# Kernel optimization log

Measured on AMD Instinct MI355X. Metric: run time of the kernel, lower is better.

The kernel has to match this reference:

```python
import jax, jax.numpy as jnp
import numpy as np

N_NODES = 50000
N_EDGES = 800000
IN_F = 256
HID = 64
N_CLASSES = 32
LEAKY_SLOPE = 0.2


def _gat_layer(x, src, dst, W, a_src, a_dst):
    # Standard single-head GAT (GraphAttentionLayer_P0 semantics):
    # h = x W; e_ij = LeakyReLU(a_src.h_j + a_dst.h_i); softmax over in-edges of i;
    # out_i = sum_j alpha_ij h_j
    h = x @ W                                        # [N, F']
    alpha_s = h @ a_src                              # [N]
    alpha_d = h @ a_dst                              # [N]
    e = jax.nn.leaky_relu(alpha_s[src] + alpha_d[dst], LEAKY_SLOPE)  # [E]
    # segment softmax over edges grouped by destination node
    m = jax.ops.segment_max(e, dst, num_segments=N_NODES)           # [N]
    m = jnp.where(jnp.isfinite(m), m, 0.0)            # empty segments -> -inf
    ex = jnp.exp(e - m[dst])                          # [E]
    denom = jax.ops.segment_sum(ex, dst, num_segments=N_NODES)       # [N]
    denom = jnp.where(denom == 0.0, 1.0, denom)
    alpha = ex / denom[dst]                           # [E]
    out = jax.ops.segment_sum(alpha[:, None] * h[src], dst, num_segments=N_NODES)
    return out                                        # [N, F']


def setup_inputs() -> dict:
    key = jax.random.key(0)
    ks = jax.random.split(key, 8)
    x = jax.random.normal(ks[0], (N_NODES, IN_F), dtype=jnp.float32)
    edge_index = jax.random.randint(ks[1], (2, N_EDGES), 0, N_NODES, dtype=jnp.int64)
    s1 = 1.0 / np.sqrt(IN_F)
    s2 = 1.0 / np.sqrt(HID)
    W1 = jax.random.uniform(ks[2], (IN_F, HID), jnp.float32, -s1, s1)
    a1_src = jax.random.uniform(ks[3], (HID,), jnp.float32, -s2, s2)
    a1_dst = jax.random.uniform(ks[4], (HID,), jnp.float32, -s2, s2)
    W2 = jax.random.uniform(ks[5], (HID, N_CLASSES), jnp.float32, -s2, s2)
    s3 = 1.0 / np.sqrt(N_CLASSES)
    a2_src = jax.random.uniform(ks[6], (N_CLASSES,), jnp.float32, -s3, s3)
    a2_dst = jax.random.uniform(ks[7], (N_CLASSES,), jnp.float32, -s3, s3)
    return {"x": x, "edge_index": edge_index, "W1": W1, "a1_src": a1_src,
            "a1_dst": a1_dst, "W2": W2, "a2_src": a2_src, "a2_dst": a2_dst}


def reference(x, edge_index, W1, a1_src, a1_dst, W2, a2_src, a2_dst):
    src, dst = edge_index[0], edge_index[1]
    h = _gat_layer(x, src, dst, W1, a1_src, a1_dst)
    h = jax.nn.relu(h)
    out = _gat_layer(h, src, dst, W2, a2_src, a2_dst)
    return out
```

## Files before the change

kernel.cpp:

```cpp
#include <hip/hip_runtime.h>
#include <math.h>

#define NN 50000
#define NE 800000
#define INF_DIM 256
#define HIDF 64
#define NC 32
#define SLOPE 0.2f


__global__ void k_zero(int* __restrict__ counts){
  int i = blockIdx.x*blockDim.x + threadIdx.x;
  if(i < NN) counts[i] = 0;
}

__global__ void k_hist(const int* __restrict__ dst, int* __restrict__ counts){
  int e = blockIdx.x*blockDim.x + threadIdx.x;
  if(e < NE) atomicAdd(&counts[dst[e]], 1);
}

__global__ void k_scan_a(const int* __restrict__ counts, int* __restrict__ rowstart,
                         int* __restrict__ blocksums){
  __shared__ int wsum[4];
  int tid = threadIdx.x;
  int idx = blockIdx.x*1024 + tid*4;
  int v0 = (idx+0<NN)?counts[idx+0]:0;
  int v1 = (idx+1<NN)?counts[idx+1]:0;
  int v2 = (idx+2<NN)?counts[idx+2]:0;
  int v3 = (idx+3<NN)?counts[idx+3]:0;
  int s0=v0, s1=s0+v1, s2=s1+v2, s3=s2+v3;
  int lane = tid & 63, w = tid >> 6;
  int x = s3;
  #pragma unroll
  for(int off=1; off<64; off<<=1){
    int y = __shfl_up(x, off, 64);
    if(lane >= off) x += y;
  }
  if(lane==63) wsum[w] = x;
  __syncthreads();
  int woff = 0;
  for(int i=0;i<w;i++) woff += wsum[i];
  int excl = woff + (x - s3);
  if(idx+0<NN) rowstart[idx+1] = excl + s0;
  if(idx+1<NN) rowstart[idx+2] = excl + s1;
  if(idx+2<NN) rowstart[idx+3] = excl + s2;
  if(idx+3<NN) rowstart[idx+4] = excl + s3;
  if(tid==0) blocksums[blockIdx.x] = wsum[0]+wsum[1]+wsum[2]+wsum[3];
}

__global__ void k_scan_b(const int* __restrict__ blocksums, int* __restrict__ blockoff){
  int lane = threadIdx.x;
  const int nb = (NN + 1023)/1024;
  int v = (lane<nb)? blocksums[lane] : 0;
  int x = v;
  #pragma unroll
  for(int off=1; off<64; off<<=1){
    int y = __shfl_up(x, off, 64);
    if(lane >= off) x += y;
  }
  if(lane<nb) blockoff[lane] = x - v;
}

__global__ void k_scan_c(const int* __restrict__ counts, int* __restrict__ rowstart,
                         const int* __restrict__ blockoff, int* __restrict__ cursor){
  int i = blockIdx.x*blockDim.x + threadIdx.x;
  if(i < NN){
    int incl = rowstart[i+1] + blockoff[i>>10];
    rowstart[i+1] = incl;
    cursor[i] = incl - counts[i];
    if(i==0) rowstart[0] = 0;
  }
}

__global__ void k_scatter(const int* __restrict__ src, const int* __restrict__ dst,
                          int* __restrict__ cursor, int* __restrict__ ssrc){
  int e = blockIdx.x*blockDim.x + threadIdx.x;
  if(e < NE){
    int d = dst[e];
    int pos = atomicAdd(&cursor[d], 1);
    ssrc[pos] = src[e];
  }
}

#define LDXS 20

__global__ __launch_bounds__(64) void k_gemm1(
    const float* __restrict__ x, const float* __restrict__ W,
    const float* __restrict__ a_s, const float* __restrict__ a_d,
    float* __restrict__ h, float* __restrict__ as_o, float* __restrict__ ad_o){
  __shared__ float xs[64*LDXS];
  __shared__ float ws[16*64];
  int tid = threadIdx.x;
  int ng = tid >> 3;
  int cg = tid & 7;
  int nb0 = blockIdx.x*64;

  int srow = nb0 + tid; if(srow > NN-1) srow = NN-1;
  const float* xrow = x + (size_t)srow*INF_DIM;
  int wrow = tid >> 2;
  int wcol = (tid & 3)*16;

  float4 xr[4], wr[4];
  #pragma unroll
  for(int j=0;j<4;j++){
    xr[j] = *reinterpret_cast<const float4*>(xrow + j*4);
    wr[j] = *reinterpret_cast<const float4*>(W + wrow*64 + wcol + j*4);
  }

  float4 acc0[8], acc1[8];
  #pragma unroll
  for(int i=0;i<8;i++){
    acc0[i] = make_float4(0.f,0.f,0.f,0.f);
    acc1[i] = make_float4(0.f,0.f,0.f,0.f);
  }

  for(int kt=0; kt<16; ++kt){
    #pragma unroll
    for(int j=0;j<4;j++){
      *reinterpret_cast<float4*>(xs + tid*LDXS + j*4) = xr[j];
      *reinterpret_cast<float4*>(ws + wrow*64 + wcol + j*4) = wr[j];
    }
    __syncthreads();
    if(kt < 15){
      #pragma unroll
      for(int j=0;j<4;j++){
        xr[j] = *reinterpret_cast<const float4*>(xrow + (kt+1)*16 + j*4);
        wr[j] = *reinterpret_cast<const float4*>(W + ((kt+1)*16 + wrow)*64 + wcol + j*4);
      }
    }
    #pragma unroll
    for(int k4=0;k4<4;k4++){
      int k = k4*4;
      float4 wa[4], wb[4];
      #pragma unroll
      for(int kk=0;kk<4;kk++){
        wa[kk] = *reinterpret_cast<const float4*>(ws + (k+kk)*64 + cg*8);
        wb[kk] = *reinterpret_cast<const float4*>(ws + (k+kk)*64 + cg*8 + 4);
      }
      #pragma unroll
      for(int i=0;i<8;i++){
        float4 xv = *reinterpret_cast<const float4*>(xs + (ng + 8*i)*LDXS + k);
        acc0[i].x += xv.x*wa[0].x + xv.y*wa[1].x + xv.z*wa[2].x + xv.w*wa[3].x;
        acc0[i].y += xv.x*wa[0].y + xv.y*wa[1].y + xv.z*wa[2].y + xv.w*wa[3].y;
        acc0[i].z += xv.x*wa[0].z + xv.y*wa[1].z + xv.z*wa[2].z + xv.w*wa[3].z;
        acc0[i].w += xv.x*wa[0].w + xv.y*wa[1].w + xv.z*wa[2].w + xv.w*wa[3].w;
        acc1[i].x += xv.x*wb[0].x + xv.y*wb[1].x + xv.z*wb[2].x + xv.w*wb[3].x;
        acc1[i].y += xv.x*wb[0].y + xv.y*wb[1].y + xv.z*wb[2].y + xv.w*wb[3].y;
        acc1[i].z += xv.x*wb[0].z + xv.y*wb[1].z + xv.z*wb[2].z + xv.w*wb[3].z;
        acc1[i].w += xv.x*wb[0].w + xv.y*wb[1].w + xv.z*wb[2].w + xv.w*wb[3].w;
      }
    }
    __syncthreads();
  }

  float4 asA = *reinterpret_cast<const float4*>(a_s + cg*8);
  float4 asB = *reinterpret_cast<const float4*>(a_s + cg*8 + 4);
  float4 adA = *reinterpret_cast<const float4*>(a_d + cg*8);
  float4 adB = *reinterpret_cast<const float4*>(a_d + cg*8 + 4);
  #pragma unroll
  for(int i=0;i<8;i++){
    int n = nb0 + ng + 8*i;
    float sv = acc0[i].x*asA.x + acc0[i].y*asA.y + acc0[i].z*asA.z + acc0[i].w*asA.w
             + acc1[i].x*asB.x + acc1[i].y*asB.y + acc1[i].z*asB.z + acc1[i].w*asB.w;
    float dv = acc0[i].x*adA.x + acc0[i].y*adA.y + acc0[i].z*adA.z + acc0[i].w*adA.w
             + acc1[i].x*adB.x + acc1[i].y*adB.y + acc1[i].z*adB.z + acc1[i].w*adB.w;
    #pragma unroll
    for(int mk=1; mk<8; mk<<=1){
      sv += __shfl_xor(sv, mk, 64);
      dv += __shfl_xor(dv, mk, 64);
    }
    if(n < NN){
      *reinterpret_cast<float4*>(h + (size_t)n*HIDF + cg*8)     = acc0[i];
      *reinterpret_cast<float4*>(h + (size_t)n*HIDF + cg*8 + 4) = acc1[i];
      if(cg==0){ as_o[n]=sv; ad_o[n]=dv; }
    }
  }
}


__global__ __launch_bounds__(256) void k_agg1(
    const float* __restrict__ h1, const float* __restrict__ as1, const float* __restrict__ ad1,
    const int* __restrict__ rowstart, const int* __restrict__ ssrc,
    float* __restrict__ r1){
  int wv = threadIdx.x >> 6;
  int lane = threadIdx.x & 63;
  int n = blockIdx.x*4 + wv;
  int rs = rowstart[n], re = rowstart[n+1];
  float adn = ad1[n];
  float m = -1e30f, l = 0.f, acc = 0.f;
  for(int base=rs; base<re; base+=64){
    int cnt = re - base; if(cnt > 64) cnt = 64;
    int s = 0; float z = -1e30f;
    if(lane < cnt){
      s = ssrc[base+lane];
      float zz = as1[s] + adn;
      z = zz > 0.f ? zz : SLOPE*zz;
    }
    float cm = z;
    #pragma unroll
    for(int off=32; off>=1; off>>=1) cm = fmaxf(cm, __shfl_xor(cm, off, 64));
    float nm = fmaxf(m, cm);
    float sc = __expf(m - nm);
    float p = (lane<cnt) ? __expf(z - nm) : 0.f;
    float cs = p;
    #pragma unroll
    for(int off=32; off>=1; off>>=1) cs += __shfl_xor(cs, off, 64);
    l = l*sc + cs;
    acc *= sc;
    for(int e=0; e<cnt; ++e){
      int   se = __shfl(s, e, 64);
      float pe = __shfl(p, e, 64);
      acc += pe * h1[(size_t)se*HIDF + lane];
    }
    m = nm;
  }
  float o = (l > 0.f) ? acc/l : 0.f;
  r1[(size_t)n*HIDF + lane] = fmaxf(o, 0.f);
}


__global__ __launch_bounds__(64) void k_gemm2(
    const float* __restrict__ r1, const float* __restrict__ W2,
    const float* __restrict__ a_s, const float* __restrict__ a_d,
    float* __restrict__ h2, float* __restrict__ as_o, float* __restrict__ ad_o){
  __shared__ float ws2[64*32];
  int tid = threadIdx.x;
  int ng = tid >> 2;
  int cg = tid & 3;
  int nb0 = blockIdx.x*128;
  #pragma unroll
  for(int j=0;j<8;j++)
    *reinterpret_cast<float4*>(ws2 + tid*32 + j*4) =
        *reinterpret_cast<const float4*>(W2 + tid*32 + j*4);
  __syncthreads();

  float4 acc0[8], acc1[8];
  #pragma unroll
  for(int i=0;i<8;i++){
    acc0[i] = make_float4(0.f,0.f,0.f,0.f);
    acc1[i] = make_float4(0.f,0.f,0.f,0.f);
  }

  float4 xc[8], xn[8];
  #pragma unroll
  for(int i=0;i<8;i++){
    int n = nb0 + ng + 16*i; if(n > NN-1) n = NN-1;
    xc[i] = *reinterpret_cast<const float4*>(r1 + (size_t)n*HIDF);
  }
  for(int k4=0;k4<16;k4++){
    if(k4 < 15){
      #pragma unroll
      for(int i=0;i<8;i++){
        int n = nb0 + ng + 16*i; if(n > NN-1) n = NN-1;
        xn[i] = *reinterpret_cast<const float4*>(r1 + (size_t)n*HIDF + (k4+1)*4);
      }
    }
    float4 wa[4], wb[4];
    #pragma unroll
    for(int kk=0;kk<4;kk++){
      wa[kk] = *reinterpret_cast<const float4*>(ws2 + (k4*4+kk)*32 + cg*8);
      wb[kk] = *reinterpret_cast<const float4*>(ws2 + (k4*4+kk)*32 + cg*8 + 4);
    }
    #pragma unroll
    for(int i=0;i<8;i++){
      float4 xv = xc[i];
      acc0[i].x += xv.x*wa[0].x + xv.y*wa[1].x + xv.z*wa[2].x + xv.w*wa[3].x;
      acc0[i].y += xv.x*wa[0].y + xv.y*wa[1].y + xv.z*wa[2].y + xv.w*wa[3].y;
      acc0[i].z += xv.x*wa[0].z + xv.y*wa[1].z + xv.z*wa[2].z + xv.w*wa[3].z;
      acc0[i].w += xv.x*wa[0].w + xv.y*wa[1].w + xv.z*wa[2].w + xv.w*wa[3].w;
      acc1[i].x += xv.x*wb[0].x + xv.y*wb[1].x + xv.z*wb[2].x + xv.w*wb[3].x;
      acc1[i].y += xv.x*wb[0].y + xv.y*wb[1].y + xv.z*wb[2].y + xv.w*wb[3].y;
      acc1[i].z += xv.x*wb[0].z + xv.y*wb[1].z + xv.z*wb[2].z + xv.w*wb[3].z;
      acc1[i].w += xv.x*wb[0].w + xv.y*wb[1].w + xv.z*wb[2].w + xv.w*wb[3].w;
    }
    #pragma unroll
    for(int i=0;i<8;i++) xc[i] = xn[i];
  }

  float4 asA = *reinterpret_cast<const float4*>(a_s + cg*8);
  float4 asB = *reinterpret_cast<const float4*>(a_s + cg*8 + 4);
  float4 adA = *reinterpret_cast<const float4*>(a_d + cg*8);
  float4 adB = *reinterpret_cast<const float4*>(a_d + cg*8 + 4);
  #pragma unroll
  for(int i=0;i<8;i++){
    int n = nb0 + ng + 16*i;
    float sv = acc0[i].x*asA.x + acc0[i].y*asA.y + acc0[i].z*asA.z + acc0[i].w*asA.w
             + acc1[i].x*asB.x + acc1[i].y*asB.y + acc1[i].z*asB.z + acc1[i].w*asB.w;
    float dv = acc0[i].x*adA.x + acc0[i].y*adA.y + acc0[i].z*adA.z + acc0[i].w*adA.w
             + acc1[i].x*adB.x + acc1[i].y*adB.y + acc1[i].z*adB.z + acc1[i].w*adB.w;
    #pragma unroll
    for(int mk=1; mk<4; mk<<=1){
      sv += __shfl_xor(sv, mk, 64);
      dv += __shfl_xor(dv, mk, 64);
    }
    if(n < NN){
      *reinterpret_cast<float4*>(h2 + (size_t)n*NC + cg*8)     = acc0[i];
      *reinterpret_cast<float4*>(h2 + (size_t)n*NC + cg*8 + 4) = acc1[i];
      if(cg==0){ as_o[n]=sv; ad_o[n]=dv; }
    }
  }
}


__global__ __launch_bounds__(256) void k_agg2(
    const float* __restrict__ h2, const float* __restrict__ as2, const float* __restrict__ ad2,
    const int* __restrict__ rowstart, const int* __restrict__ ssrc,
    float* __restrict__ out){
  int tid = threadIdx.x;
  int sub = tid >> 5;
  int c = tid & 31;
  int n = blockIdx.x*8 + sub;
  int rs = rowstart[n], re = rowstart[n+1];
  float adn = ad2[n];
  float m = -1e30f, l = 0.f, acc = 0.f;
  for(int base=rs; base<re; base+=32){
    int cnt = re - base; if(cnt > 32) cnt = 32;
    int s = 0; float z = -1e30f;
    if(c < cnt){
      s = ssrc[base+c];
      float zz = as2[s] + adn;
      z = zz > 0.f ? zz : SLOPE*zz;
    }
    float cm = z;
    #pragma unroll
    for(int off=16; off>=1; off>>=1) cm = fmaxf(cm, __shfl_xor(cm, off, 32));
    float nm = fmaxf(m, cm);
    float sc = __expf(m - nm);
    float p = (c<cnt) ? __expf(z - nm) : 0.f;
    float cs = p;
    #pragma unroll
    for(int off=16; off>=1; off>>=1) cs += __shfl_xor(cs, off, 32);
    l = l*sc + cs;
    acc *= sc;
    for(int e=0; e<cnt; ++e){
      int   se = __shfl(s, e, 32);
      float pe = __shfl(p, e, 32);
      acc += pe * h2[(size_t)se*NC + c];
    }
    m = nm;
  }
  out[(size_t)n*NC + c] = (l > 0.f) ? acc/l : 0.f;
}


extern "C" void kernel_launch(void* const* d_in, const int* in_sizes, int n_in,
                              void* d_out, int out_size, void* d_ws, size_t ws_size,
                              hipStream_t stream){
  const float* x   = (const float*)d_in[0];
  const int*   ei  = (const int*)d_in[1];
  const float* W1  = (const float*)d_in[2];
  const float* a1s = (const float*)d_in[3];
  const float* a1d = (const float*)d_in[4];
  const float* W2  = (const float*)d_in[5];
  const float* a2s = (const float*)d_in[6];
  const float* a2d = (const float*)d_in[7];
  const int* srcIdx = ei;
  const int* dstIdx = ei + NE;
  float* out = (float*)d_out;

  char* wsp = (char*)d_ws;
  size_t off = 0;
  auto alloc = [&](size_t bytes)->void*{
    void* p = wsp + off;
    off = (off + bytes + 255) & ~(size_t)255;
    return p;
  };
  int* counts    = (int*)alloc((size_t)NN*sizeof(int));
  int* rowstart  = (int*)alloc((size_t)(NN+1)*sizeof(int));
  int* cursor    = (int*)alloc((size_t)NN*sizeof(int));
  int* blocksums = (int*)alloc(64*sizeof(int));
  int* blockoff  = (int*)alloc(64*sizeof(int));
  int* ssrc      = (int*)alloc((size_t)NE*sizeof(int));
  float* h1      = (float*)alloc((size_t)NN*HIDF*sizeof(float));
  float* as1     = (float*)alloc((size_t)NN*sizeof(float));
  float* ad1     = (float*)alloc((size_t)NN*sizeof(float));
  float* r1      = (float*)alloc((size_t)NN*HIDF*sizeof(float));
  float* h2  = h1;
  float* as2 = as1;
  float* ad2 = ad1;

  k_zero   <<<(NN+255)/256, 256, 0, stream>>>(counts);
  k_hist   <<<(NE+255)/256, 256, 0, stream>>>(dstIdx, counts);
  k_scan_a <<<(NN+1023)/1024, 256, 0, stream>>>(counts, rowstart, blocksums);
  k_scan_b <<<1, 64, 0, stream>>>(blocksums, blockoff);
  k_scan_c <<<(NN+255)/256, 256, 0, stream>>>(counts, rowstart, blockoff, cursor);
  k_scatter<<<(NE+255)/256, 256, 0, stream>>>(srcIdx, dstIdx, cursor, ssrc);

  k_gemm1<<<(NN+63)/64, 64, 0, stream>>>(x, W1, a1s, a1d, h1, as1, ad1);
  k_agg1 <<<NN/4, 256, 0, stream>>>(h1, as1, ad1, rowstart, ssrc, r1);

  k_gemm2<<<(NN+127)/128, 64, 0, stream>>>(r1, W2, a2s, a2d, h2, as2, ad2);
  k_agg2 <<<NN/8, 256, 0, stream>>>(h2, as2, ad2, rowstart, ssrc, out);
}
```

Before: 362.5 us.

## Use one-row-per-thread GEMMs with uniform weight loads; stage edge pairs in LDS

Both projection GEMMs are rewritten so each thread computes a full output row, reading weights through wave-uniform global loads instead of staging x and W tiles in shared memory with barriers. The attention dot products are then done in-thread with no shuffles. In the aggregation kernels, the per-edge (source, weight) pairs are written to shared memory and read back as broadcasts, replacing two cross-lane shuffles per edge. The risks are uncoalesced strided row loads of x (each lane reads a different 1 KB row), high register pressure from 64 accumulators, and a missing barrier. The LDS write and reads happen within a single wavefront, so this relies on wave-level ordering.

Measured after the change: 351.5 us. -3.1%, faster.

```diff
diff --git a/kernel.cpp b/kernel.cpp
--- a/kernel.cpp
+++ b/kernel.cpp
@@ -82,98 +82,65 @@
   }
 }
 
-#define LDXS 20
 
 __global__ __launch_bounds__(64) void k_gemm1(
     const float* __restrict__ x, const float* __restrict__ W,
     const float* __restrict__ a_s, const float* __restrict__ a_d,
     float* __restrict__ h, float* __restrict__ as_o, float* __restrict__ ad_o){
-  __shared__ float xs[64*LDXS];
-  __shared__ float ws[16*64];
-  int tid = threadIdx.x;
-  int ng = tid >> 3;
-  int cg = tid & 7;
-  int nb0 = blockIdx.x*64;
-
-  int srow = nb0 + tid; if(srow > NN-1) srow = NN-1;
-  const float* xrow = x + (size_t)srow*INF_DIM;
-  int wrow = tid >> 2;
-  int wcol = (tid & 3)*16;
-
-  float4 xr[4], wr[4];
-  #pragma unroll
-  for(int j=0;j<4;j++){
-    xr[j] = *reinterpret_cast<const float4*>(xrow + j*4);
-    wr[j] = *reinterpret_cast<const float4*>(W + wrow*64 + wcol + j*4);
-  }
-
-  float4 acc0[8], acc1[8];
-  #pragma unroll
-  for(int i=0;i<8;i++){
-    acc0[i] = make_float4(0.f,0.f,0.f,0.f);
-    acc1[i] = make_float4(0.f,0.f,0.f,0.f);
-  }
+  int lane = threadIdx.x;
+  int n = blockIdx.x*64 + lane;
+  int nr = (n < NN) ? n : (NN-1);
+  const float* xrow = x + (size_t)nr*INF_DIM;
+  const float4* Wv = reinterpret_cast<const float4*>(W);
+
+  float4 acc[16];
+  #pragma unroll
+  for(int i=0;i<16;i++) acc[i] = make_float4(0.f,0.f,0.f,0.f);
+
+  float4 xc[4], xn[4];
+  #pragma unroll
+  for(int j=0;j<4;j++) xc[j] = *reinterpret_cast<const float4*>(xrow + j*4);
 
   for(int kt=0; kt<16; ++kt){
-    #pragma unroll
-    for(int j=0;j<4;j++){
-      *reinterpret_cast<float4*>(xs + tid*LDXS + j*4) = xr[j];
-      *reinterpret_cast<float4*>(ws + wrow*64 + wcol + j*4) = wr[j];
-    }
-    __syncthreads();
     if(kt < 15){
       #pragma unroll
-      for(int j=0;j<4;j++){
-        xr[j] = *reinterpret_cast<const float4*>(xrow + (kt+1)*16 + j*4);
-        wr[j] = *reinterpret_cast<const float4*>(W + ((kt+1)*16 + wrow)*64 + wcol + j*4);
+      for(int j=0;j<4;j++)
+        xn[j] = *reinterpret_cast<const float4*>(xrow + (kt+1)*16 + j*4);
+    }
+    #pragma unroll
+    for(int k4=0;k4<4;k4++){
+      int kbase = kt*16 + k4*4;
+      float4 xk = xc[k4];
+      #pragma unroll
+      for(int cb=0;cb<16;cb++){
+        float4 w0 = Wv[(kbase+0)*16 + cb];
+        float4 w1 = Wv[(kbase+1)*16 + cb];
+        float4 w2 = Wv[(kbase+2)*16 + cb];
+        float4 w3 = Wv[(kbase+3)*16 + cb];
+        acc[cb].x += xk.x*w0.x + xk.y*w1.x + xk.z*w2.x + xk.w*w3.x;
+        acc[cb].y += xk.x*w0.y + xk.y*w1.y + xk.z*w2.y + xk.w*w3.y;
+        acc[cb].z += xk.x*w0.z + xk.y*w1.z + xk.z*w2.z + xk.w*w3.z;
+        acc[cb].w += xk.x*w0.w + xk.y*w1.w + xk.z*w2.w + xk.w*w3.w;
       }
     }
     #pragma unroll
-    for(int k4=0;k4<4;k4++){
-      int k = k4*4;
-      float4 wa[4], wb[4];
-      #pragma unroll
-      for(int kk=0;kk<4;kk++){
-        wa[kk] = *reinterpret_cast<const float4*>(ws + (k+kk)*64 + cg*8);
-        wb[kk] = *reinterpret_cast<const float4*>(ws + (k+kk)*64 + cg*8 + 4);
-      }
-      #pragma unroll
-      for(int i=0;i<8;i++){
-        float4 xv = *reinterpret_cast<const float4*>(xs + (ng + 8*i)*LDXS + k);
-        acc0[i].x += xv.x*wa[0].x + xv.y*wa[1].x + xv.z*wa[2].x + xv.w*wa[3].x;
-        acc0[i].y += xv.x*wa[0].y + xv.y*wa[1].y + xv.z*wa[2].y + xv.w*wa[3].y;
-        acc0[i].z += xv.x*wa[0].z + xv.y*wa[1].z + xv.z*wa[2].z + xv.w*wa[3].z;
-        acc0[i].w += xv.x*wa[0].w + xv.y*wa[1].w + xv.z*wa[2].w + xv.w*wa[3].w;
-        acc1[i].x += xv.x*wb[0].x + xv.y*wb[1].x + xv.z*wb[2].x + xv.w*wb[3].x;
-        acc1[i].y += xv.x*wb[0].y + xv.y*wb[1].y + xv.z*wb[2].y + xv.w*wb[3].y;
-        acc1[i].z += xv.x*wb[0].z + xv.y*wb[1].z + xv.z*wb[2].z + xv.w*wb[3].z;
-        acc1[i].w += xv.x*wb[0].w + xv.y*wb[1].w + xv.z*wb[2].w + xv.w*wb[3].w;
-      }
-    }
-    __syncthreads();
-  }
-
-  float4 asA = *reinterpret_cast<const float4*>(a_s + cg*8);
-  float4 asB = *reinterpret_cast<const float4*>(a_s + cg*8 + 4);
-  float4 adA = *reinterpret_cast<const float4*>(a_d + cg*8);
-  float4 adB = *reinterpret_cast<const float4*>(a_d + cg*8 + 4);
-  #pragma unroll
-  for(int i=0;i<8;i++){
-    int n = nb0 + ng + 8*i;
-    float sv = acc0[i].x*asA.x + acc0[i].y*asA.y + acc0[i].z*asA.z + acc0[i].w*asA.w
-             + acc1[i].x*asB.x + acc1[i].y*asB.y + acc1[i].z*asB.z + acc1[i].w*asB.w;
-    float dv = acc0[i].x*adA.x + acc0[i].y*adA.y + acc0[i].z*adA.z + acc0[i].w*adA.w
-             + acc1[i].x*adB.x + acc1[i].y*adB.y + acc1[i].z*adB.z + acc1[i].w*adB.w;
-    #pragma unroll
-    for(int mk=1; mk<8; mk<<=1){
-      sv += __shfl_xor(sv, mk, 64);
-      dv += __shfl_xor(dv, mk, 64);
-    }
-    if(n < NN){
-      *reinterpret_cast<float4*>(h + (size_t)n*HIDF + cg*8)     = acc0[i];
-      *reinterpret_cast<float4*>(h + (size_t)n*HIDF + cg*8 + 4) = acc1[i];
-      if(cg==0){ as_o[n]=sv; ad_o[n]=dv; }
-    }
+    for(int j=0;j<4;j++) xc[j] = xn[j];
+  }
+
+  const float4* asv = reinterpret_cast<const float4*>(a_s);
+  const float4* adv = reinterpret_cast<const float4*>(a_d);
+  float sv = 0.f, dv = 0.f;
+  #pragma unroll
+  for(int cb=0;cb<16;cb++){
+    float4 a4 = asv[cb], d4 = adv[cb];
+    sv += acc[cb].x*a4.x + acc[cb].y*a4.y + acc[cb].z*a4.z + acc[cb].w*a4.w;
+    dv += acc[cb].x*d4.x + acc[cb].y*d4.y + acc[cb].z*d4.z + acc[cb].w*d4.w;
+  }
+  if(n < NN){
+    #pragma unroll
+    for(int cb=0;cb<16;cb++)
+      *reinterpret_cast<float4*>(h + (size_t)n*HIDF + cb*4) = acc[cb];
+    as_o[n] = sv; ad_o[n] = dv;
   }
 }
 
@@ -182,6 +149,7 @@
     const float* __restrict__ h1, const float* __restrict__ as1, const float* __restrict__ ad1,
     const int* __restrict__ rowstart, const int* __restrict__ ssrc,
     float* __restrict__ r1){
+  __shared__ int2 sp[4][64];
   int wv = threadIdx.x >> 6;
   int lane = threadIdx.x & 63;
   int n = blockIdx.x*4 + wv;
@@ -207,10 +175,10 @@
     for(int off=32; off>=1; off>>=1) cs += __shfl_xor(cs, off, 64);
     l = l*sc + cs;
     acc *= sc;
+    sp[wv][lane] = make_int2(s, __float_as_int(p));
     for(int e=0; e<cnt; ++e){
-      int   se = __shfl(s, e, 64);
-      float pe = __shfl(p, e, 64);
-      acc += pe * h1[(size_t)se*HIDF + lane];
+      int2 v = sp[wv][e];
+      acc += __int_as_float(v.y) * h1[(size_t)v.x*HIDF + lane];
     }
     m = nm;
   }
@@ -223,81 +191,60 @@
     const float* __restrict__ r1, const float* __restrict__ W2,
     const float* __restrict__ a_s, const float* __restrict__ a_d,
     float* __restrict__ h2, float* __restrict__ as_o, float* __restrict__ ad_o){
-  __shared__ float ws2[64*32];
-  int tid = threadIdx.x;
-  int ng = tid >> 2;
-  int cg = tid & 3;
-  int nb0 = blockIdx.x*128;
-  #pragma unroll
-  for(int j=0;j<8;j++)
-    *reinterpret_cast<float4*>(ws2 + tid*32 + j*4) =
-        *reinterpret_cast<const float4*>(W2 + tid*32 + j*4);
-  __syncthreads();
-
-  float4 acc0[8], acc1[8];
-  #pragma unroll
-  for(int i=0;i<8;i++){
-    acc0[i] = make_float4(0.f,0.f,0.f,0.f);
-    acc1[i] = make_float4(0.f,0.f,0.f,0.f);
-  }
-
-  float4 xc[8], xn[8];
-  #pragma unroll
-  for(int i=0;i<8;i++){
-    int n = nb0 + ng + 16*i; if(n > NN-1) n = NN-1;
-    xc[i] = *reinterpret_cast<const float4*>(r1 + (size_t)n*HIDF);
-  }
-  for(int k4=0;k4<16;k4++){
-    if(k4 < 15){
+  int lane = threadIdx.x;
+  int n = blockIdx.x*64 + lane;
+  int nr = (n < NN) ? n : (NN-1);
+  const float* xrow = r1 + (size_t)nr*HIDF;
+  const float4* Wv = reinterpret_cast<const float4*>(W2);
+
+  float4 acc[8];
+  #pragma unroll
+  for(int i=0;i<8;i++) acc[i] = make_float4(0.f,0.f,0.f,0.f);
+
+  float4 xc[4], xn[4];
+  #pragma unroll
+  for(int j=0;j<4;j++) xc[j] = *reinterpret_cast<const float4*>(xrow + j*4);
+
+  for(int kt=0; kt<4; ++kt){
+    if(kt < 3){
       #pragma unroll
-      for(int i=0;i<8;i++){
-        int n = nb0 + ng + 16*i; if(n > NN-1) n = NN-1;
-        xn[i] = *reinterpret_cast<const float4*>(r1 + (size_t)n*HIDF + (k4+1)*4);
+      for(int j=0;j<4;j++)
+        xn[j] = *reinterpret_cast<const float4*>(xrow + (kt+1)*16 + j*4);
+    }
+    #pragma unroll
+    for(int k4=0;k4<4;k4++){
+      int kbase = kt*16 + k4*4;
+      float4 xk = xc[k4];
+      #pragma unroll
+      for(int cb=0;cb<8;cb++){
+        float4 w0 = Wv[(kbase+0)*8 + cb];
+        float4 w1 = Wv[(kbase+1)*8 + cb];
+        float4 w2 = Wv[(kbase+2)*8 + cb];
+        float4 w3 = Wv[(kbase+3)*8 + cb];
+        acc[cb].x += xk.x*w0.x + xk.y*w1.x + xk.z*w2.x + xk.w*w3.x;
+        acc[cb].y += xk.x*w0.y + xk.y*w1.y + xk.z*w2.y + xk.w*w3.y;
+        acc[cb].z += xk.x*w0.z + xk.y*w1.z + xk.z*w2.z + xk.w*w3.z;
+        acc[cb].w += xk.x*w0.w + xk.y*w1.w + xk.z*w2.w + xk.w*w3.w;
       }
     }
-    float4 wa[4], wb[4];
-    #pragma unroll
-    for(int kk=0;kk<4;kk++){
-      wa[kk] = *reinterpret_cast<const float4*>(ws2 + (k4*4+kk)*32 + cg*8);
-      wb[kk] = *reinterpret_cast<const float4*>(ws2 + (k4*4+kk)*32 + cg*8 + 4);
-    }
-    #pragma unroll
-    for(int i=0;i<8;i++){
-      float4 xv = xc[i];
-      acc0[i].x += xv.x*wa[0].x + xv.y*wa[1].x + xv.z*wa[2].x + xv.w*wa[3].x;
-      acc0[i].y += xv.x*wa[0].y + xv.y*wa[1].y + xv.z*wa[2].y + xv.w*wa[3].y;
-      acc0[i].z += xv.x*wa[0].z + xv.y*wa[1].z + xv.z*wa[2].z + xv.w*wa[3].z;
-      acc0[i].w += xv.x*wa[0].w + xv.y*wa[1].w + xv.z*wa[2].w + xv.w*wa[3].w;
-      acc1[i].x += xv.x*wb[0].x + xv.y*wb[1].x + xv.z*wb[2].x + xv.w*wb[3].x;
-      acc1[i].y += xv.x*wb[0].y + xv.y*wb[1].y + xv.z*wb[2].y + xv.w*wb[3].y;
-      acc1[i].z += xv.x*wb[0].z + xv.y*wb[1].z + xv.z*wb[2].z + xv.w*wb[3].z;
-      acc1[i].w += xv.x*wb[0].w + xv.y*wb[1].w + xv.z*wb[2].w + xv.w*wb[3].w;
-    }
-    #pragma unroll
-    for(int i=0;i<8;i++) xc[i] = xn[i];
-  }
-
-  float4 asA = *reinterpret_cast<const float4*>(a_s + cg*8);
-  float4 asB = *reinterpret_cast<const float4*>(a_s + cg*8 + 4);
-  float4 adA = *reinterpret_cast<const float4*>(a_d + cg*8);
-  float4 adB = *reinterpret_cast<const float4*>(a_d + cg*8 + 4);
-  #pragma unroll
-  for(int i=0;i<8;i++){
-    int n = nb0 + ng + 16*i;
-    float sv = acc0[i].x*asA.x + acc0[i].y*asA.y + acc0[i].z*asA.z + acc0[i].w*asA.w
-             + acc1[i].x*asB.x + acc1[i].y*asB.y + acc1[i].z*asB.z + acc1[i].w*asB.w;
-    float dv = acc0[i].x*adA.x + acc0[i].y*adA.y + acc0[i].z*adA.z + acc0[i].w*adA.w
-             + acc1[i].x*adB.x + acc1[i].y*adB.y + acc1[i].z*adB.z + acc1[i].w*adB.w;
-    #pragma unroll
-    for(int mk=1; mk<4; mk<<=1){
-      sv += __shfl_xor(sv, mk, 64);
-      dv += __shfl_xor(dv, mk, 64);
-    }
-    if(n < NN){
-      *reinterpret_cast<float4*>(h2 + (size_t)n*NC + cg*8)     = acc0[i];
-      *reinterpret_cast<float4*>(h2 + (size_t)n*NC + cg*8 + 4) = acc1[i];
-      if(cg==0){ as_o[n]=sv; ad_o[n]=dv; }
-    }
+    #pragma unroll
+    for(int j=0;j<4;j++) xc[j] = xn[j];
+  }
+
+  const float4* asv = reinterpret_cast<const float4*>(a_s);
+  const float4* adv = reinterpret_cast<const float4*>(a_d);
+  float sv = 0.f, dv = 0.f;
+  #pragma unroll
+  for(int cb=0;cb<8;cb++){
+    float4 a4 = asv[cb], d4 = adv[cb];
+    sv += acc[cb].x*a4.x + acc[cb].y*a4.y + acc[cb].z*a4.z + acc[cb].w*a4.w;
+    dv += acc[cb].x*d4.x + acc[cb].y*d4.y + acc[cb].z*d4.z + acc[cb].w*d4.w;
+  }
+  if(n < NN){
+    #pragma unroll
+    for(int cb=0;cb<8;cb++)
+      *reinterpret_cast<float4*>(h2 + (size_t)n*NC + cb*4) = acc[cb];
+    as_o[n] = sv; ad_o[n] = dv;
   }
 }
 
@@ -306,6 +253,7 @@
     const float* __restrict__ h2, const float* __restrict__ as2, const float* __restrict__ ad2,
     const int* __restrict__ rowstart, const int* __restrict__ ssrc,
     float* __restrict__ out){
+  __shared__ int2 sp2[8][32];
   int tid = threadIdx.x;
   int sub = tid >> 5;
   int c = tid & 31;
@@ -332,10 +280,10 @@
     for(int off=16; off>=1; off>>=1) cs += __shfl_xor(cs, off, 32);
     l = l*sc + cs;
     acc *= sc;
+    sp2[sub][c] = make_int2(s, __float_as_int(p));
     for(int e=0; e<cnt; ++e){
-      int   se = __shfl(s, e, 32);
-      float pe = __shfl(p, e, 32);
-      acc += pe * h2[(size_t)se*NC + c];
+      int2 v = sp2[sub][e];
+      acc += __int_as_float(v.y) * h2[(size_t)v.x*NC + c];
     }
     m = nm;
   }
@@ -389,6 +337,6 @@
   k_gemm1<<<(NN+63)/64, 64, 0, stream>>>(x, W1, a1s, a1d, h1, as1, ad1);
   k_agg1 <<<NN/4, 256, 0, stream>>>(h1, as1, ad1, rowstart, ssrc, r1);
 
-  k_gemm2<<<(NN+127)/128, 64, 0, stream>>>(r1, W2, a2s, a2d, h2, as2, ad2);
+  k_gemm2<<<(NN+63)/64, 64, 0, stream>>>(r1, W2, a2s, a2d, h2, as2, ad2);
   k_agg2 <<<NN/8, 256, 0, stream>>>(h2, as2, ad2, rowstart, ssrc, out);
 }
```
